# Kernel optimization log

Measured on AMD Instinct MI355X. Metric: run time of the kernel, lower is better.

## Reference

```python
import jax, jax.numpy as jnp
import numpy as np

N = 100_000      # nodes
E = 1_600_000    # edges (avg degree 16)
IN = 128
H = 128
OUT = 2
G = 512          # graphs in the batch


def setup_inputs() -> dict:
    key = jax.random.key(0)
    ks = jax.random.split(key, 10)
    x = jax.random.normal(ks[0], (N, IN), dtype=jnp.float32)
    edge_index = jax.random.randint(ks[1], (2, E), 0, N, dtype=jnp.int64)
    edge_weight = jax.random.uniform(ks[2], (E,), dtype=jnp.float32)
    batch = jnp.sort(jax.random.randint(ks[3], (N,), 0, G, dtype=jnp.int64))
    s_in = 1.0 / np.sqrt(IN)
    s_h = 1.0 / np.sqrt(H)
    W1 = jax.random.normal(ks[4], (IN, H), dtype=jnp.float32) * s_in
    b1 = jnp.zeros((H,), dtype=jnp.float32)
    W2 = jax.random.normal(ks[5], (H, H), dtype=jnp.float32) * s_h
    b2 = jnp.zeros((H,), dtype=jnp.float32)
    Wl = jax.random.normal(ks[6], (H, OUT), dtype=jnp.float32) * s_h
    bl = jnp.zeros((OUT,), dtype=jnp.float32)
    return {"x": x, "edge_index": edge_index, "edge_weight": edge_weight,
            "batch": batch, "W1": W1, "b1": b1, "W2": W2, "b2": b2,
            "Wl": Wl, "bl": bl}


def _gcn_layer(x, W, b, row, col, ew, n):
    # PyG GCNConv: linear transform, symmetric-normalized scatter-add, bias.
    xw = x @ W                                           # [n, H]
    deg = jax.ops.segment_sum(ew, col, num_segments=n)    # weighted in-degree
    dis = jnp.where(deg > 0, jax.lax.rsqrt(deg), 0.0)
    norm = dis[row] * ew * dis[col]                       # [E+n]
    msg = xw[row] * norm[:, None]                         # gather + scale
    out = jax.ops.segment_sum(msg, col, num_segments=n)   # scatter-add to targets
    return out + b


def reference(x, edge_index, edge_weight, batch, W1, b1, W2, b2, Wl, bl):
    n = x.shape[0]
    # GCNConv default: add self-loops with weight 1.0 (gcn_norm fill_value=1)
    loop = jnp.arange(n, dtype=edge_index.dtype)
    row = jnp.concatenate([edge_index[0], loop])
    col = jnp.concatenate([edge_index[1], loop])
    ew = jnp.concatenate([edge_weight, jnp.ones((n,), edge_weight.dtype)])

    h = jax.nn.relu(_gcn_layer(x, W1, b1, row, col, ew, n))
    h = jax.nn.relu(_gcn_layer(h, W2, b2, row, col, ew, n))

    # global_mean_pool over batch ids
    cnt = jax.ops.segment_sum(jnp.ones((n,), h.dtype), batch, num_segments=G)
    pooled = jax.ops.segment_sum(h, batch, num_segments=G)
    pooled = pooled / jnp.maximum(cnt, 1.0)[:, None]      # [G, H]

    return pooled @ Wl + bl                               # [G, OUT]
```

## Files before the change

### kernel.cpp

```cpp
#include <hip/hip_runtime.h>
#include <hip/hip_fp16.h>


#define HDIM 128
typedef unsigned int uint;
typedef _Float16 half8 __attribute__((ext_vector_type(8)));
typedef float f32x4 __attribute__((ext_vector_type(4)));
typedef float f32x2 __attribute__((ext_vector_type(2)));

template <typename AT>
__device__ __forceinline__ void gemm_body(
    const AT* __restrict__ A, const float* __restrict__ W,
    unsigned char* __restrict__ Y, int n, int nstrip, int tid, int bid,
    int nblk, char* smem) {
  char* Wt = smem;
  for (int t = tid; t < 2048; t += 256) {
    int c = t & 127;
    int k8 = t >> 7;
    const float* wp = W + (size_t)(k8 * 8) * HDIM + c;
    half8 hv;
#pragma unroll
    for (int m = 0; m < 8; ++m) hv[m] = (_Float16)wp[m * HDIM];
    int byte = c * 256 + k8 * 16;
    byte ^= ((c & 7) << 4);
    *(half8*)&Wt[byte] = hv;
  }
  __syncthreads();

  int wave = tid >> 6, lane = tid & 63;
  int l15 = lane & 15, l4 = lane >> 4;
  char* ep = smem + 32768 + wave * 2048;
  int stride = nblk * 4;
  for (int s = bid * 4 + wave; s < nstrip; s += stride) {
    int row0 = s << 4;
    int xrl = min(row0 + l15, n - 1);
    half8 bf[4];
    if constexpr (sizeof(AT) == 4) {
      const float* ap = (const float*)A + (size_t)xrl * HDIM + l4 * 8;
#pragma unroll
      for (int kk = 0; kk < 4; ++kk) {
        float4 u = *(const float4*)(ap + kk * 32);
        float4 v = *(const float4*)(ap + kk * 32 + 4);
        half8 h;
        h[0] = (_Float16)u.x; h[1] = (_Float16)u.y;
        h[2] = (_Float16)u.z; h[3] = (_Float16)u.w;
        h[4] = (_Float16)v.x; h[5] = (_Float16)v.y;
        h[6] = (_Float16)v.z; h[7] = (_Float16)v.w;
        bf[kk] = h;
      }
    } else {
      const half8* ap = (const half8*)((const _Float16*)A + (size_t)xrl * HDIM + l4 * 8);
#pragma unroll
      for (int kk = 0; kk < 4; ++kk) bf[kk] = ap[kk * 4];
    }
    f32x4 acc[8];
#pragma unroll
    for (int cf = 0; cf < 8; ++cf) acc[cf] = (f32x4){0.f, 0.f, 0.f, 0.f};
#pragma unroll
    for (int kk = 0; kk < 4; ++kk) {
#pragma unroll
      for (int cf = 0; cf < 8; ++cf) {
        int c = cf * 16 + l15;
        int byte = c * 256 + kk * 64 + l4 * 16;
        byte ^= ((c & 7) << 4);
        half8 af = *(half8*)&Wt[byte];
        acc[cf] = __builtin_amdgcn_mfma_f32_16x16x32_f16(af, bf[kk], acc[cf], 0, 0, 0);
      }
    }
#pragma unroll
    for (int cf = 0; cf < 8; ++cf) {
      int w = 0;
      w = __builtin_amdgcn_cvt_pk_fp8_f32(acc[cf][0], acc[cf][1], w, false);
      w = __builtin_amdgcn_cvt_pk_fp8_f32(acc[cf][2], acc[cf][3], w, true);
      int byte = l15 * 128 + ((cf * 16) ^ ((l15 & 7) << 4)) + l4 * 4;
      *(int*)&ep[byte] = w;
    }
    asm volatile("s_waitcnt lgkmcnt(0)" ::: "memory");
#pragma unroll
    for (int p = 0; p < 2; ++p) {
      int rl = p * 8 + (lane >> 3);
      int c16 = (lane & 7) * 16;
      int byte = rl * 128 + (c16 ^ ((rl & 7) << 4));
      uint4 v = *(uint4*)&ep[byte];
      int orow = row0 + rl;
      if (orow < n)
        *(uint4*)(Y + (size_t)orow * 128 + c16) = v;
    }
  }
}

__global__ __launch_bounds__(256) void gemm1_hist_kernel(
    const float* __restrict__ A, const float* __restrict__ W,
    unsigned char* __restrict__ Y, int n, int nstrip, int MBg,
    const int* __restrict__ col, const float* __restrict__ ew,
    uint* __restrict__ dc32, unsigned char* __restrict__ rank, int E, int HB) {
  __shared__ __align__(16) char smem[40960];
  int bid = blockIdx.x;
  if (bid & 1) {
    gemm_body<float>(A, W, Y, n, nstrip, threadIdx.x, bid >> 1, MBg, smem);
    return;
  }
  int stride = HB * 256;
  for (int e = (bid >> 1) * 256 + threadIdx.x; e < E; e += 4 * stride) {
#pragma unroll
    for (int q = 0; q < 4; ++q) {
      int eq = e + q * stride;
      if (eq < E) {
        int c = col[eq];
        uint pack = (1u << 26) + __float2uint_rn(ew[eq] * 65536.0f);
        uint old = atomicAdd(&dc32[(size_t)c * 4], pack);
        rank[eq] = (unsigned char)(old >> 26);
      }
    }
  }
}

__global__ __launch_bounds__(256) void gemm_mfma_kernel(
    const _Float16* __restrict__ A, const float* __restrict__ W,
    unsigned char* __restrict__ Y, int n, int nstrip) {
  __shared__ __align__(16) char smem[40960];
  gemm_body<_Float16>(A, W, Y, n, nstrip, threadIdx.x, blockIdx.x, gridDim.x, smem);
}

__global__ __launch_bounds__(256) void node_scan_kernel(
    const uint* __restrict__ dc32, float* __restrict__ dis,
    const int* __restrict__ batch, int* __restrict__ start,
    int* __restrict__ off, int* __restrict__ part, int n, int G) {
  __shared__ int tmp[256];
  int tid = threadIdx.x;
  int i = blockIdx.x * 256 + tid;
  int v = 0;
  if (i < n) {
    uint p = dc32[(size_t)i * 4];
    v = (int)(p >> 26);
    float deg = (float)(p & 0x3FFFFFFu) * (1.0f / 65536.0f);
    dis[i] = rsqrtf(deg + 1.0f);
    int b = batch[i];
    if (i == 0) {
      for (int h = 0; h <= b; ++h) start[h] = 0;
    } else {
      int bp = batch[i - 1];
      for (int h = bp + 1; h <= b; ++h) start[h] = i;
    }
    if (i == n - 1) {
      for (int h = b + 1; h <= G; ++h) start[h] = n;
    }
  }
  tmp[tid] = v;
  __syncthreads();
  for (int d = 1; d < 256; d <<= 1) {
    int t = (tid >= d) ? tmp[tid - d] : 0;
    __syncthreads();
    tmp[tid] += t;
    __syncthreads();
  }
  if (i < n) off[i] = tmp[tid] - v;
  if (tid == 255) part[blockIdx.x] = tmp[255];
}

__global__ __launch_bounds__(512) void scan_part_kernel(int* part, int nb) {
  __shared__ int tmp[512];
  int tid = threadIdx.x;
  int v = (tid < nb) ? part[tid] : 0;
  tmp[tid] = v;
  __syncthreads();
  for (int d = 1; d < 512; d <<= 1) {
    int t = (tid >= d) ? tmp[tid - d] : 0;
    __syncthreads();
    tmp[tid] += t;
    __syncthreads();
  }
  if (tid < nb) part[tid] = tmp[tid] - v;
}

__global__ __launch_bounds__(256) void scan_add_kernel(
    int* __restrict__ off, const int* __restrict__ part, int n, int total) {
  int i = blockIdx.x * 256 + threadIdx.x;
  if (i < n) off[i] += part[blockIdx.x];
  if (i == 0) off[n] = total;
}

__global__ __launch_bounds__(256) void fill_kernel(
    const int* __restrict__ row, const int* __restrict__ col,
    const float* __restrict__ ew, const unsigned char* __restrict__ rank,
    const float* __restrict__ dis, const int* __restrict__ off,
    uint* __restrict__ csr, int E) {
  int e = blockIdx.x * 256 + threadIdx.x;
  if (e < E) {
    int c = col[e];
    int r = row[e];
    int slot = off[c] + (int)rank[e];
    uint nq = __float2uint_rn(dis[r] * ew[e] * 32768.0f);
    nq = min(nq, 32767u);
    csr[slot] = ((uint)r << 15) | nq;
  }
}

__global__ __launch_bounds__(256) void agg_kernel(
    const uint* __restrict__ xw, const uint* __restrict__ csr,
    const float* __restrict__ dis, const int* __restrict__ off,
    const float* __restrict__ bias, uint* __restrict__ out, int n) {
  int node = blockIdx.x * 4 + (threadIdx.x >> 6);
  if (node >= n) return;
  int lane = threadIdx.x & 63;
  int hl = lane & 31;
  int par = lane >> 5;
  float dc = dis[node];
  float a0, a1, a2, a3;
  {
    uint v = xw[(size_t)node * 32 + hl];
    f32x2 lo = __builtin_amdgcn_cvt_pk_f32_fp8((int)v, false);
    f32x2 hi = __builtin_amdgcn_cvt_pk_f32_fp8((int)v, true);
    float sd = (par == 0) ? dc : 0.0f;
    a0 = sd * lo[0]; a1 = sd * lo[1]; a2 = sd * hi[0]; a3 = sd * hi[1];
  }
  const float qs = 1.0f / 32768.0f;
  int s = off[node], t = off[node + 1];
  int i = s;
  for (; i + 8 <= t; i += 8) {
    uint e0 = csr[i + par];
    uint e1 = csr[i + 2 + par];
    uint e2 = csr[i + 4 + par];
    uint e3 = csr[i + 6 + par];
    uint v0 = xw[(size_t)(e0 >> 15) * 32 + hl];
    uint v1 = xw[(size_t)(e1 >> 15) * 32 + hl];
    uint v2 = xw[(size_t)(e2 >> 15) * 32 + hl];
    uint v3 = xw[(size_t)(e3 >> 15) * 32 + hl];
    float n0 = (float)(e0 & 0x7FFFu) * qs;
    float n1 = (float)(e1 & 0x7FFFu) * qs;
    float n2 = (float)(e2 & 0x7FFFu) * qs;
    float n3 = (float)(e3 & 0x7FFFu) * qs;
    f32x2 l0 = __builtin_amdgcn_cvt_pk_f32_fp8((int)v0, false);
    f32x2 h0 = __builtin_amdgcn_cvt_pk_f32_fp8((int)v0, true);
    f32x2 l1 = __builtin_amdgcn_cvt_pk_f32_fp8((int)v1, false);
    f32x2 h1 = __builtin_amdgcn_cvt_pk_f32_fp8((int)v1, true);
    f32x2 l2 = __builtin_amdgcn_cvt_pk_f32_fp8((int)v2, false);
    f32x2 h2 = __builtin_amdgcn_cvt_pk_f32_fp8((int)v2, true);
    f32x2 l3 = __builtin_amdgcn_cvt_pk_f32_fp8((int)v3, false);
    f32x2 h3 = __builtin_amdgcn_cvt_pk_f32_fp8((int)v3, true);
    a0 += n0 * l0[0]; a1 += n0 * l0[1]; a2 += n0 * h0[0]; a3 += n0 * h0[1];
    a0 += n1 * l1[0]; a1 += n1 * l1[1]; a2 += n1 * h1[0]; a3 += n1 * h1[1];
    a0 += n2 * l2[0]; a1 += n2 * l2[1]; a2 += n2 * h2[0]; a3 += n2 * h2[1];
    a0 += n3 * l3[0]; a1 += n3 * l3[1]; a2 += n3 * h3[0]; a3 += n3 * h3[1];
  }
  for (; i < t; i += 2) {
    if (i + par < t) {
      uint e = csr[i + par];
      uint v = xw[(size_t)(e >> 15) * 32 + hl];
      float nn = (float)(e & 0x7FFFu) * qs;
      f32x2 lo = __builtin_amdgcn_cvt_pk_f32_fp8((int)v, false);
      f32x2 hi = __builtin_amdgcn_cvt_pk_f32_fp8((int)v, true);
      a0 += nn * lo[0]; a1 += nn * lo[1]; a2 += nn * hi[0]; a3 += nn * hi[1];
    }
  }
  a0 += __shfl_xor(a0, 32);
  a1 += __shfl_xor(a1, 32);
  a2 += __shfl_xor(a2, 32);
  a3 += __shfl_xor(a3, 32);
  if (par == 0) {
    float4 b = *(const float4*)(bias + hl * 4);
    a0 = fmaxf(dc * a0 + b.x, 0.0f);
    a1 = fmaxf(dc * a1 + b.y, 0.0f);
    a2 = fmaxf(dc * a2 + b.z, 0.0f);
    a3 = fmaxf(dc * a3 + b.w, 0.0f);
    __half2 p0 = __floats2half2_rn(a0, a1);
    __half2 p1 = __floats2half2_rn(a2, a3);
    ((uint2*)out)[(size_t)node * 32 + hl] = make_uint2(*(uint*)&p0, *(uint*)&p1);
  }
}

__global__ __launch_bounds__(256) void pool_kernel(
    const uint* __restrict__ h, const int* __restrict__ start,
    float* __restrict__ pooled) {
  __shared__ float2 red[256];
  int g = blockIdx.x;
  int grp = threadIdx.x >> 6, f = threadIdx.x & 63;
  int s = start[g], e = start[g + 1];
  float s0 = 0.0f, s1 = 0.0f;
  for (int r = s + grp; r < e; r += 4) {
    uint v = h[((size_t)r << 6) + f];
    float2 fv = __half22float2(*(const __half2*)&v);
    s0 += fv.x;
    s1 += fv.y;
  }
  red[threadIdx.x] = make_float2(s0, s1);
  __syncthreads();
  if (grp == 0) {
    float2 a = red[f], b = red[64 + f], c = red[128 + f], d = red[192 + f];
    float inv = 1.0f / (float)max(e - s, 1);
    pooled[g * HDIM + 2 * f]     = (a.x + b.x + c.x + d.x) * inv;
    pooled[g * HDIM + 2 * f + 1] = (a.y + b.y + c.y + d.y) * inv;
  }
}

__global__ __launch_bounds__(64) void final_kernel(
    const float* __restrict__ pooled, const float* __restrict__ Wl,
    const float* __restrict__ bl, float* __restrict__ out) {
  int g = blockIdx.x;
  int lane = threadIdx.x;
  float p0 = pooled[g * HDIM + lane];
  float p1 = pooled[g * HDIM + 64 + lane];
#pragma unroll
  for (int o = 0; o < 2; ++o) {
    float s = p0 * Wl[lane * 2 + o] + p1 * Wl[(64 + lane) * 2 + o];
    for (int d = 32; d > 0; d >>= 1) s += __shfl_down(s, d);
    if (lane == 0) out[g * 2 + o] = s + bl[o];
  }
}

extern "C" void kernel_launch(void* const* d_in, const int* in_sizes, int n_in,
                              void* d_out, int out_size, void* d_ws, size_t ws_size,
                              hipStream_t stream) {
  const float* x     = (const float*)d_in[0];
  const int*   ei    = (const int*)d_in[1];
  const float* ew    = (const float*)d_in[2];
  const int*   batch = (const int*)d_in[3];
  const float* W1    = (const float*)d_in[4];
  const float* b1    = (const float*)d_in[5];
  const float* W2    = (const float*)d_in[6];
  const float* b2    = (const float*)d_in[7];
  const float* Wl    = (const float*)d_in[8];
  const float* bl    = (const float*)d_in[9];
  float* out = (float*)d_out;

  const int N = in_sizes[0] / HDIM;
  const int E = in_sizes[2];
  const int G = out_size / 2;

  const int* row = ei;
  const int* col = ei + E;

  auto al = [](size_t v) { return (v + 255) & ~(size_t)255; };
  char* ws = (char*)d_ws;
  size_t o_dc32   = 0;
  size_t zero_end = o_dc32   + al((size_t)N * 16);
  size_t o_rank   = zero_end;
  size_t o_dis    = o_rank   + al((size_t)E);
  size_t o_start  = o_dis    + al((size_t)N * 4);
  size_t o_off    = o_start  + al(((size_t)G + 1) * 4);
  size_t o_part   = o_off    + al(((size_t)N + 1) * 4);
  size_t o_csr    = o_part   + al(2048);
  size_t o_xw     = o_csr    + al((size_t)E * 4);
  size_t o_h      = o_xw     + al((size_t)N * 128);
  size_t o_pooled = o_h      + al((size_t)N * 64 * 4);

  uint*  dc32    = (uint*) (ws + o_dc32);
  unsigned char* rank = (unsigned char*)(ws + o_rank);
  float* dis     = (float*)(ws + o_dis);
  int*   start   = (int*)  (ws + o_start);
  int*   off     = (int*)  (ws + o_off);
  int*   part    = (int*)  (ws + o_part);
  uint*  csr     = (uint*) (ws + o_csr);
  unsigned char* xw = (unsigned char*)(ws + o_xw);
  uint*  hbuf    = (uint*) (ws + o_h);
  float* pooled  = (float*)(ws + o_pooled);

  hipMemsetAsync(ws, 0, zero_end, stream);

  int EB = (E + 255) / 256;
  int NB = (N + 255) / 256;
  int nstrip = (N + 15) / 16;
  int MBg = 1024;
  int HB  = 1024;
  int MB  = 1024;
  int AB  = (N + 3) / 4;

  gemm1_hist_kernel<<<MBg + HB, 256, 0, stream>>>(
      x, W1, xw, N, nstrip, MBg, col, ew, dc32, rank, E, HB);

  node_scan_kernel<<<NB, 256, 0, stream>>>(dc32, dis, batch, start, off, part, N, G);
  scan_part_kernel<<<1, 512, 0, stream>>>(part, NB);
  scan_add_kernel<<<NB, 256, 0, stream>>>(off, part, N, E);

  fill_kernel<<<EB, 256, 0, stream>>>(row, col, ew, rank, dis, off, csr, E);

  agg_kernel<<<AB, 256, 0, stream>>>((const uint*)xw, csr, dis, off, b1, hbuf, N);

  gemm_mfma_kernel<<<MB, 256, 0, stream>>>((const _Float16*)hbuf, W2, xw, N, nstrip);
  agg_kernel<<<AB, 256, 0, stream>>>((const uint*)xw, csr, dis, off, b2, hbuf, N);

  pool_kernel<<<G, 256, 0, stream>>>(hbuf, start, pooled);
  final_kernel<<<G, 64, 0, stream>>>(pooled, Wl, bl, out);
}
```

Before: 247.1 us.

## Use decoupled look-back scan, fuse pool with final linear, deepen agg unroll

Replaces the three-kernel offset scan (block scan, partial scan, add) with a single-pass decoupled look-back scan that keeps per-block descriptors in zeroed workspace. Merges the pooling and final linear kernels so the pooled vector never goes through global memory. Raises the aggregation loop's gather batch from 4 to 8 edges per lane to put more independent loads in flight. This cuts kernel launches and small serial kernels, but the look-back spin assumes earlier blocks make progress, and the wider unroll uses more registers.

```diff
diff --git a/kernel.cpp b/kernel.cpp
--- a/kernel.cpp
+++ b/kernel.cpp
@@ -4,6 +4,7 @@
 
 #define HDIM 128
 typedef unsigned int uint;
+typedef unsigned long long u64;
 typedef _Float16 half8 __attribute__((ext_vector_type(8)));
 typedef float f32x4 __attribute__((ext_vector_type(4)));
 typedef float f32x2 __attribute__((ext_vector_type(2)));
@@ -125,25 +126,28 @@
 __global__ __launch_bounds__(256) void node_scan_kernel(
     const uint* __restrict__ dc32, float* __restrict__ dis,
     const int* __restrict__ batch, int* __restrict__ start,
-    int* __restrict__ off, int* __restrict__ part, int n, int G) {
+    int* __restrict__ off, u64* __restrict__ desc, int n, int G, int E) {
   __shared__ int tmp[256];
+  __shared__ int exs;
   int tid = threadIdx.x;
-  int i = blockIdx.x * 256 + tid;
+  int b = blockIdx.x;
+  int i = b * 256 + tid;
   int v = 0;
   if (i < n) {
     uint p = dc32[(size_t)i * 4];
     v = (int)(p >> 26);
     float deg = (float)(p & 0x3FFFFFFu) * (1.0f / 65536.0f);
     dis[i] = rsqrtf(deg + 1.0f);
-    int b = batch[i];
+    int bb = batch[i];
     if (i == 0) {
-      for (int h = 0; h <= b; ++h) start[h] = 0;
+      for (int h = 0; h <= bb; ++h) start[h] = 0;
+      off[n] = E;
     } else {
       int bp = batch[i - 1];
-      for (int h = bp + 1; h <= b; ++h) start[h] = i;
+      for (int h = bp + 1; h <= bb; ++h) start[h] = i;
     }
     if (i == n - 1) {
-      for (int h = b + 1; h <= G; ++h) start[h] = n;
+      for (int h = bb + 1; h <= G; ++h) start[h] = n;
     }
   }
   tmp[tid] = v;
@@ -154,30 +158,28 @@
     tmp[tid] += t;
     __syncthreads();
   }
-  if (i < n) off[i] = tmp[tid] - v;
-  if (tid == 255) part[blockIdx.x] = tmp[255];
-}
-
-__global__ __launch_bounds__(512) void scan_part_kernel(int* part, int nb) {
-  __shared__ int tmp[512];
-  int tid = threadIdx.x;
-  int v = (tid < nb) ? part[tid] : 0;
-  tmp[tid] = v;
+  if (tid == 0) {
+    u64 agg = (u64)(uint)tmp[255];
+    int ex = 0;
+    if (b == 0) {
+      atomicExch(&desc[0], (2ull << 62) | agg);
+    } else {
+      atomicExch(&desc[b], (1ull << 62) | agg);
+      int p = b - 1;
+      while (true) {
+        u64 s = atomicAdd(&desc[p], 0ull);
+        u64 fl = s >> 62;
+        if (fl == 0) continue;
+        ex += (int)(uint)s;
+        if (fl == 2) break;
+        --p;
+      }
+      atomicExch(&desc[b], (2ull << 62) | (u64)(uint)(ex + tmp[255]));
+    }
+    exs = ex;
+  }
   __syncthreads();
-  for (int d = 1; d < 512; d <<= 1) {
-    int t = (tid >= d) ? tmp[tid - d] : 0;
-    __syncthreads();
-    tmp[tid] += t;
-    __syncthreads();
-  }
-  if (tid < nb) part[tid] = tmp[tid] - v;
-}
-
-__global__ __launch_bounds__(256) void scan_add_kernel(
-    int* __restrict__ off, const int* __restrict__ part, int n, int total) {
-  int i = blockIdx.x * 256 + threadIdx.x;
-  if (i < n) off[i] += part[blockIdx.x];
-  if (i == 0) off[n] = total;
+  if (i < n) off[i] = exs + tmp[tid] - v;
 }
 
 __global__ __launch_bounds__(256) void fill_kernel(
@@ -217,31 +219,35 @@
   const float qs = 1.0f / 32768.0f;
   int s = off[node], t = off[node + 1];
   int i = s;
+  for (; i + 16 <= t; i += 16) {
+    uint ee[8];
+#pragma unroll
+    for (int j = 0; j < 8; ++j) ee[j] = csr[i + 2 * j + par];
+    uint vv[8];
+#pragma unroll
+    for (int j = 0; j < 8; ++j) vv[j] = xw[(size_t)(ee[j] >> 15) * 32 + hl];
+#pragma unroll
+    for (int j = 0; j < 8; ++j) {
+      float nn = (float)(ee[j] & 0x7FFFu) * qs;
+      f32x2 lo = __builtin_amdgcn_cvt_pk_f32_fp8((int)vv[j], false);
+      f32x2 hi = __builtin_amdgcn_cvt_pk_f32_fp8((int)vv[j], true);
+      a0 += nn * lo[0]; a1 += nn * lo[1]; a2 += nn * hi[0]; a3 += nn * hi[1];
+    }
+  }
   for (; i + 8 <= t; i += 8) {
-    uint e0 = csr[i + par];
-    uint e1 = csr[i + 2 + par];
-    uint e2 = csr[i + 4 + par];
-    uint e3 = csr[i + 6 + par];
-    uint v0 = xw[(size_t)(e0 >> 15) * 32 + hl];
-    uint v1 = xw[(size_t)(e1 >> 15) * 32 + hl];
-    uint v2 = xw[(size_t)(e2 >> 15) * 32 + hl];
-    uint v3 = xw[(size_t)(e3 >> 15) * 32 + hl];
-    float n0 = (float)(e0 & 0x7FFFu) * qs;
-    float n1 = (float)(e1 & 0x7FFFu) * qs;
-    float n2 = (float)(e2 & 0x7FFFu) * qs;
-    float n3 = (float)(e3 & 0x7FFFu) * qs;
-    f32x2 l0 = __builtin_amdgcn_cvt_pk_f32_fp8((int)v0, false);
-    f32x2 h0 = __builtin_amdgcn_cvt_pk_f32_fp8((int)v0, true);
-    f32x2 l1 = __builtin_amdgcn_cvt_pk_f32_fp8((int)v1, false);
-    f32x2 h1 = __builtin_amdgcn_cvt_pk_f32_fp8((int)v1, true);
-    f32x2 l2 = __builtin_amdgcn_cvt_pk_f32_fp8((int)v2, false);
-    f32x2 h2 = __builtin_amdgcn_cvt_pk_f32_fp8((int)v2, true);
-    f32x2 l3 = __builtin_amdgcn_cvt_pk_f32_fp8((int)v3, false);
-    f32x2 h3 = __builtin_amdgcn_cvt_pk_f32_fp8((int)v3, true);
-    a0 += n0 * l0[0]; a1 += n0 * l0[1]; a2 += n0 * h0[0]; a3 += n0 * h0[1];
-    a0 += n1 * l1[0]; a1 += n1 * l1[1]; a2 += n1 * h1[0]; a3 += n1 * h1[1];
-    a0 += n2 * l2[0]; a1 += n2 * l2[1]; a2 += n2 * h2[0]; a3 += n2 * h2[1];
-    a0 += n3 * l3[0]; a1 += n3 * l3[1]; a2 += n3 * h3[0]; a3 += n3 * h3[1];
+    uint ee[4];
+#pragma unroll
+    for (int j = 0; j < 4; ++j) ee[j] = csr[i + 2 * j + par];
+    uint vv[4];
+#pragma unroll
+    for (int j = 0; j < 4; ++j) vv[j] = xw[(size_t)(ee[j] >> 15) * 32 + hl];
+#pragma unroll
+    for (int j = 0; j < 4; ++j) {
+      float nn = (float)(ee[j] & 0x7FFFu) * qs;
+      f32x2 lo = __builtin_amdgcn_cvt_pk_f32_fp8((int)vv[j], false);
+      f32x2 hi = __builtin_amdgcn_cvt_pk_f32_fp8((int)vv[j], true);
+      a0 += nn * lo[0]; a1 += nn * lo[1]; a2 += nn * hi[0]; a3 += nn * hi[1];
+    }
   }
   for (; i < t; i += 2) {
     if (i + par < t) {
@@ -269,9 +275,10 @@
   }
 }
 
-__global__ __launch_bounds__(256) void pool_kernel(
+__global__ __launch_bounds__(256) void pool_final_kernel(
     const uint* __restrict__ h, const int* __restrict__ start,
-    float* __restrict__ pooled) {
+    const float* __restrict__ Wl, const float* __restrict__ bl,
+    float* __restrict__ out) {
   __shared__ float2 red[256];
   int g = blockIdx.x;
   int grp = threadIdx.x >> 6, f = threadIdx.x & 63;
@@ -288,23 +295,14 @@
   if (grp == 0) {
     float2 a = red[f], b = red[64 + f], c = red[128 + f], d = red[192 + f];
     float inv = 1.0f / (float)max(e - s, 1);
-    pooled[g * HDIM + 2 * f]     = (a.x + b.x + c.x + d.x) * inv;
-    pooled[g * HDIM + 2 * f + 1] = (a.y + b.y + c.y + d.y) * inv;
-  }
-}
-
-__global__ __launch_bounds__(64) void final_kernel(
-    const float* __restrict__ pooled, const float* __restrict__ Wl,
-    const float* __restrict__ bl, float* __restrict__ out) {
-  int g = blockIdx.x;
-  int lane = threadIdx.x;
-  float p0 = pooled[g * HDIM + lane];
-  float p1 = pooled[g * HDIM + 64 + lane];
-#pragma unroll
-  for (int o = 0; o < 2; ++o) {
-    float s = p0 * Wl[lane * 2 + o] + p1 * Wl[(64 + lane) * 2 + o];
-    for (int d = 32; d > 0; d >>= 1) s += __shfl_down(s, d);
-    if (lane == 0) out[g * 2 + o] = s + bl[o];
+    float pv0 = (a.x + b.x + c.x + d.x) * inv;
+    float pv1 = (a.y + b.y + c.y + d.y) * inv;
+#pragma unroll
+    for (int o = 0; o < 2; ++o) {
+      float sdot = pv0 * Wl[4 * f + o] + pv1 * Wl[4 * f + 2 + o];
+      for (int d2 = 32; d2 > 0; d2 >>= 1) sdot += __shfl_down(sdot, d2);
+      if (f == 0) out[g * 2 + o] = sdot + bl[o];
+    }
   }
 }
 
@@ -333,27 +331,25 @@
   auto al = [](size_t v) { return (v + 255) & ~(size_t)255; };
   char* ws = (char*)d_ws;
   size_t o_dc32   = 0;
-  size_t zero_end = o_dc32   + al((size_t)N * 16);
+  size_t o_desc   = o_dc32   + al((size_t)N * 16);
+  size_t zero_end = o_desc   + al(4096);
   size_t o_rank   = zero_end;
   size_t o_dis    = o_rank   + al((size_t)E);
   size_t o_start  = o_dis    + al((size_t)N * 4);
   size_t o_off    = o_start  + al(((size_t)G + 1) * 4);
-  size_t o_part   = o_off    + al(((size_t)N + 1) * 4);
-  size_t o_csr    = o_part   + al(2048);
+  size_t o_csr    = o_off    + al(((size_t)N + 1) * 4);
   size_t o_xw     = o_csr    + al((size_t)E * 4);
   size_t o_h      = o_xw     + al((size_t)N * 128);
-  size_t o_pooled = o_h      + al((size_t)N * 64 * 4);
 
   uint*  dc32    = (uint*) (ws + o_dc32);
+  u64*   desc    = (u64*)  (ws + o_desc);
   unsigned char* rank = (unsigned char*)(ws + o_rank);
   float* dis     = (float*)(ws + o_dis);
   int*   start   = (int*)  (ws + o_start);
   int*   off     = (int*)  (ws + o_off);
-  int*   part    = (int*)  (ws + o_part);
   uint*  csr     = (uint*) (ws + o_csr);
   unsigned char* xw = (unsigned char*)(ws + o_xw);
   uint*  hbuf    = (uint*) (ws + o_h);
-  float* pooled  = (float*)(ws + o_pooled);
 
   hipMemsetAsync(ws, 0, zero_end, stream);
 
@@ -368,9 +364,8 @@
   gemm1_hist_kernel<<<MBg + HB, 256, 0, stream>>>(
       x, W1, xw, N, nstrip, MBg, col, ew, dc32, rank, E, HB);
 
-  node_scan_kernel<<<NB, 256, 0, stream>>>(dc32, dis, batch, start, off, part, N, G);
-  scan_part_kernel<<<1, 512, 0, stream>>>(part, NB);
-  scan_add_kernel<<<NB, 256, 0, stream>>>(off, part, N, E);
+  node_scan_kernel<<<NB, 256, 0, stream>>>(dc32, dis, batch, start, off, desc,
+                                           N, G, E);
 
   fill_kernel<<<EB, 256, 0, stream>>>(row, col, ew, rank, dis, off, csr, E);
 
@@ -379,6 +374,5 @@
   gemm_mfma_kernel<<<MB, 256, 0, stream>>>((const _Float16*)hbuf, W2, xw, N, nstrip);
   agg_kernel<<<AB, 256, 0, stream>>>((const uint*)xw, csr, dis, off, b2, hbuf, N);
 
-  pool_kernel<<<G, 256, 0, stream>>>(hbuf, start, pooled);
-  final_kernel<<<G, 64, 0, stream>>>(pooled, Wl, bl, out);
-}
+  pool_final_kernel<<<G, 256, 0, stream>>>(hbuf, start, Wl, bl, out);
+}
```

Result: no change. 245.9 us (-0.5%).
